# Kernel optimization log

Hardware: AMD Instinct MI355X
Metric: run time of the kernel (lower is better)

The kernel has to match this reference:

```python
import jax, jax.numpy as jnp
import numpy as np

N, E, B = 50000, 800000, 64
IN, H, OUT = 64, 128, 64


def _gcn_norm(edge_index, num_nodes):
    # PyG gcn_norm with add_self_loops=True: A_hat = A + I, norm = d^-1/2[src]*d^-1/2[dst]
    loop = jnp.arange(num_nodes)
    src = jnp.concatenate([edge_index[0], loop])
    dst = jnp.concatenate([edge_index[1], loop])
    deg = jax.ops.segment_sum(jnp.ones_like(dst, dtype=jnp.float32), dst,
                              num_segments=num_nodes)  # >= 1 due to self-loops
    dis = deg ** -0.5
    norm = dis[src] * dis[dst]  # [E+N]
    return src, dst, norm


def _gcn_layer(x, W, b, src, dst, norm, num_nodes):
    h = x @ W                                   # linear first (GCNConv order)
    msg = h[src] * norm[:, None]                # gather + normalize, [E+N, H]
    out = jax.ops.segment_sum(msg, dst, num_segments=num_nodes)  # scatter-add
    return out + b


def setup_inputs() -> dict:
    key = jax.random.key(0)
    ks = jax.random.split(key, 12)
    x = jax.random.normal(ks[0], (N, IN), dtype=jnp.float32)
    edge_index = jax.random.randint(ks[1], (2, E), 0, N, dtype=jnp.int64)
    batch = jnp.sort(jax.random.randint(ks[2], (N,), 0, B, dtype=jnp.int64))

    def lin(k, fan_in, fan_out):
        s = 1.0 / np.sqrt(fan_in)
        return jax.random.uniform(k, (fan_in, fan_out), jnp.float32, -s, s)

    return {
        "x": x, "edge_index": edge_index, "batch": batch,
        "W1": lin(ks[3], IN, H), "b1": jnp.zeros((H,), jnp.float32),
        "W2": lin(ks[4], H, H),  "b2": jnp.zeros((H,), jnp.float32),
        "W3": lin(ks[5], H, H),  "b3": jnp.zeros((H,), jnp.float32),
        "W4": lin(ks[6], H, OUT), "b4": jnp.zeros((OUT,), jnp.float32),
    }


def reference(x, edge_index, batch, W1, b1, W2, b2, W3, b3, W4, b4):
    src, dst, norm = _gcn_norm(edge_index, N)
    h = jax.nn.relu(_gcn_layer(x, W1, b1, src, dst, norm, N))
    h = jax.nn.relu(_gcn_layer(h, W2, b2, src, dst, norm, N))
    # global mean pool over graphs
    sums = jax.ops.segment_sum(h, batch, num_segments=B)          # [B, H]
    cnts = jax.ops.segment_sum(jnp.ones((N,), jnp.float32), batch, num_segments=B)
    pooled = sums / jnp.maximum(cnts, 1.0)[:, None]
    # MLP head
    return jax.nn.relu(pooled @ W3 + b3) @ W4 + b4                # [B, OUT]
```

## Files before the change

### kernel.cpp

```cpp
#include <hip/hip_runtime.h>


__device__ __forceinline__ float ldf(const void* p, long long i, int f32) {
    if (f32) return ((const float*)p)[i];
    unsigned int u = ((const unsigned short*)p)[i];
    return __uint_as_float(u << 16);
}
__device__ __forceinline__ float bfl(unsigned int u) { return __uint_as_float(u << 16); }
__device__ __forceinline__ float bfh(unsigned int u) { return __uint_as_float(u & 0xFFFF0000u); }
__device__ __forceinline__ int ld_idx(const int* p, long long i, int i64) {
    return i64 ? p[2 * i] : p[i];
}
__device__ __forceinline__ unsigned short f2bf(float v) {
    unsigned int x = __float_as_uint(v);
    return (unsigned short)((x + 0x7FFFu + ((x >> 16) & 1u)) >> 16);
}
__device__ __forceinline__ int clampi(int v, int lo, int hi) {
    return v < lo ? lo : (v > hi ? hi : v);
}


__global__ void gnn_detect(const unsigned int* __restrict__ w1_words,
                           const int* __restrict__ ei_words,
                           int* __restrict__ flags) {
    __shared__ int cnt;
    __shared__ int orred;
    int t = threadIdx.x;
    if (t == 0) { cnt = 0; orred = 0; }
    __syncthreads();
    int c = 0, o = 0;
    for (int i = t; i < 512; i += 256) {
        unsigned int e = (w1_words[i] >> 7) & 0xFFu;
        if (e >= 100 && e <= 140) c++;
    }
    for (int i = t; i < 4096; i += 256) o |= ei_words[2 * i + 1];
    atomicAdd(&cnt, c);
    atomicOr(&orred, o);
    __syncthreads();
    if (t == 0) {
        flags[0] = (cnt > 256) ? 0 : 1;
        flags[1] = (orred == 0) ? 1 : 0;
    }
}


__global__ void gnn_zeroall(int* __restrict__ degcnt, int* __restrict__ fillcnt,
                            float* __restrict__ pooled, float* __restrict__ cntf,
                            int N, int B) {
    int i = blockIdx.x * 256 + threadIdx.x;
    int stride = gridDim.x * 256;
    for (int j = i; j < N; j += stride) { degcnt[j] = 0; fillcnt[j] = 0; }
    for (int j = i; j < B * 128; j += stride) pooled[j] = 0.f;
    for (int j = i; j < B; j += stride) cntf[j] = 0.f;
}

#define OW1 0
#define OB1 8192
#define OW2 8320
#define OB2 24704
#define OW3 24832
#define OB3 41216
#define OW4 41344
#define OB4 49536
#define OTOT 49600

__global__ void gnn_convert_w(const void* W1, const void* b1, const void* W2, const void* b2,
                              const void* W3, const void* b3, const void* W4, const void* b4,
                              const int* __restrict__ flags, float* __restrict__ dst) {
    int f32 = flags[0];
    int i = blockIdx.x * blockDim.x + threadIdx.x;
    if (i >= OTOT) return;
    float v;
    if      (i < OB1) v = ldf(W1, i - OW1, f32);
    else if (i < OW2) v = ldf(b1, i - OB1, f32);
    else if (i < OB2) v = ldf(W2, i - OW2, f32);
    else if (i < OW3) v = ldf(b2, i - OB2, f32);
    else if (i < OB3) v = ldf(W3, i - OW3, f32);
    else if (i < OW4) v = ldf(b3, i - OB3, f32);
    else if (i < OB4) v = ldf(W4, i - OW4, f32);
    else              v = ldf(b4, i - OB4, f32);
    dst[i] = v;
}

__global__ void gnn_convert_x(const void* __restrict__ x, const int* __restrict__ flags,
                              unsigned short* __restrict__ xb, int n64) {
    if (!flags[0]) return;
    int i = blockIdx.x * 256 + threadIdx.x;
    if (i < n64) xb[i] = f2bf(((const float*)x)[i]);
}


__global__ void gnn_hist(const int* __restrict__ ei, int E, int N,
                         const int* __restrict__ flags, int* __restrict__ degcnt) {
    int base = (blockIdx.x * 256 + threadIdx.x) * 4;
    if (base >= E) return;
    int i64 = flags[1];
    int m = min(4, E - base);
    int d[4];
#pragma unroll
    for (int j = 0; j < 4; ++j)
        if (j < m) d[j] = clampi(ld_idx(ei, (long long)E + base + j, i64), 0, N - 1);
#pragma unroll
    for (int j = 0; j < 4; ++j)
        if (j < m) atomicAdd(&degcnt[d[j]], 1);
}

__global__ void gnn_scan1(const int* __restrict__ cnt, int* __restrict__ excl,
                          int* __restrict__ sums, float* __restrict__ dis, int N) {
    __shared__ int sh[256];
    int t = threadIdx.x;
    int i = blockIdx.x * 256 + t;
    int v = (i < N) ? cnt[i] : 0;
    sh[t] = v;
    __syncthreads();
    for (int off = 1; off < 256; off <<= 1) {
        int a = (t >= off) ? sh[t - off] : 0;
        __syncthreads();
        sh[t] += a;
        __syncthreads();
    }
    if (i < N) {
        excl[i] = sh[t] - v;
        dis[i] = rsqrtf((float)v + 1.0f);
    }
    if (t == 255) sums[blockIdx.x] = sh[255];
}

__global__ void gnn_scan2(int* __restrict__ sums, int nb) {
    __shared__ int sh[256];
    int t = threadIdx.x;
    int v = (t < nb) ? sums[t] : 0;
    sh[t] = v;
    __syncthreads();
    for (int off = 1; off < 256; off <<= 1) {
        int a = (t >= off) ? sh[t - off] : 0;
        __syncthreads();
        sh[t] += a;
        __syncthreads();
    }
    if (t < nb) sums[t] = sh[t] - v;
}

__global__ void gnn_scan3(int* __restrict__ row_ptr, const int* __restrict__ sums,
                          int N, int E) {
    int i = blockIdx.x * 256 + threadIdx.x;
    if (i < N) row_ptr[i] += sums[blockIdx.x];
    if (i == 0) row_ptr[N] = E;
}

__global__ void gnn_fill(const int* __restrict__ ei, const float* __restrict__ dis,
                         const int* __restrict__ row_ptr, int* __restrict__ fillcnt,
                         int2* __restrict__ csr, int E, int N, const int* __restrict__ flags) {
    int base = (blockIdx.x * 256 + threadIdx.x) * 4;
    if (base >= E) return;
    int i64 = flags[1];
    int m = min(4, E - base);
    int s[4], d[4];
    float ws[4], wd[4];
    int pos[4];
#pragma unroll
    for (int j = 0; j < 4; ++j)
        if (j < m) {
            s[j] = clampi(ld_idx(ei, (long long)base + j, i64), 0, N - 1);
            d[j] = clampi(ld_idx(ei, (long long)E + base + j, i64), 0, N - 1);
        }
#pragma unroll
    for (int j = 0; j < 4; ++j)
        if (j < m) { ws[j] = dis[s[j]]; wd[j] = dis[d[j]]; }
#pragma unroll
    for (int j = 0; j < 4; ++j)
        if (j < m) pos[j] = row_ptr[d[j]] + atomicAdd(&fillcnt[d[j]], 1);
#pragma unroll
    for (int j = 0; j < 4; ++j)
        if (j < m) csr[pos[j]] = make_int2(s[j], __float_as_int(ws[j] * wd[j]));
}


__global__ __launch_bounds__(256) void gnn_agg_x(const void* __restrict__ x,
                                                 const unsigned short* __restrict__ xconv,
                                                 const int* __restrict__ rp,
                                                 const int2* __restrict__ csr,
                                                 const float* __restrict__ dis,
                                                 const int* __restrict__ flags,
                                                 float* __restrict__ aggX, int N) {
    const unsigned int* tab = flags[0] ? (const unsigned int*)xconv : (const unsigned int*)x;
    int t = threadIdx.x;
    int lane = t & 63;
    int n = blockIdx.x * 8 + (t >> 6) * 2 + (lane >> 5);
    if (n >= N) return;
    int fl = lane & 31;
    float dn = dis[n];
    float dn2 = dn * dn;
    unsigned int us = tab[(long long)n * 32 + fl];
    float a0 = bfl(us) * dn2, a1 = bfh(us) * dn2;
    int beg = rp[n], end = rp[n + 1];
    int e = beg;
    for (; e + 4 <= end; e += 4) {
        int2 c0 = csr[e], c1 = csr[e + 1], c2 = csr[e + 2], c3 = csr[e + 3];
        unsigned int u0 = tab[(long long)c0.x * 32 + fl];
        unsigned int u1 = tab[(long long)c1.x * 32 + fl];
        unsigned int u2 = tab[(long long)c2.x * 32 + fl];
        unsigned int u3 = tab[(long long)c3.x * 32 + fl];
        float w0 = __int_as_float(c0.y), w1 = __int_as_float(c1.y);
        float w2 = __int_as_float(c2.y), w3 = __int_as_float(c3.y);
        a0 = fmaf(w0, bfl(u0), a0); a1 = fmaf(w0, bfh(u0), a1);
        a0 = fmaf(w1, bfl(u1), a0); a1 = fmaf(w1, bfh(u1), a1);
        a0 = fmaf(w2, bfl(u2), a0); a1 = fmaf(w2, bfh(u2), a1);
        a0 = fmaf(w3, bfl(u3), a0); a1 = fmaf(w3, bfh(u3), a1);
    }
    for (; e < end; ++e) {
        int2 c = csr[e];
        unsigned int u = tab[(long long)c.x * 32 + fl];
        float w = __int_as_float(c.y);
        a0 = fmaf(w, bfl(u), a0); a1 = fmaf(w, bfh(u), a1);
    }
    *(float2*)(aggX + (long long)n * 64 + fl * 2) = make_float2(a0, a1);
}


template <int K, bool RELU, bool OUTBF>
__global__ __launch_bounds__(256) void gnn_linear(const float* __restrict__ X,
                                                  const float* __restrict__ Wf,
                                                  const float* __restrict__ bias,
                                                  int N, void* __restrict__ out) {
    __shared__ float Wl[64 * 128];
    __shared__ float Xs[32 * K];
    const int t = threadIdx.x;
    const int nbase = blockIdx.x * 32;

#pragma unroll
    for (int it = 0; it < K / 32; ++it) {
        int i4 = t + it * 256;
        int n = nbase + (i4 * 4) / K;
        float4 v = make_float4(0.f, 0.f, 0.f, 0.f);
        if (n < N) v = ((const float4*)X)[(long long)nbase * (K / 4) + i4];
        ((float4*)Xs)[i4] = v;
    }

    const int fg = t & 31, ng = t >> 5;
    const int f0 = fg * 4, n0 = ng * 4;
    float4 acc[4];
#pragma unroll
    for (int j = 0; j < 4; ++j) acc[j] = make_float4(0.f, 0.f, 0.f, 0.f);

    for (int kc = 0; kc < K; kc += 64) {
        __syncthreads();
#pragma unroll
        for (int it = 0; it < 8; ++it) {
            int i4 = t + it * 256;
            ((float4*)Wl)[i4] = ((const float4*)(Wf + kc * 128))[i4];
        }
        __syncthreads();
#pragma unroll 4
        for (int k = 0; k < 64; ++k) {
            const float4 w = *(const float4*)&Wl[k * 128 + f0];
#pragma unroll
            for (int j = 0; j < 4; ++j) {
                float xv = Xs[(n0 + j) * K + kc + k];
                acc[j].x = fmaf(xv, w.x, acc[j].x);
                acc[j].y = fmaf(xv, w.y, acc[j].y);
                acc[j].z = fmaf(xv, w.z, acc[j].z);
                acc[j].w = fmaf(xv, w.w, acc[j].w);
            }
        }
    }

#pragma unroll
    for (int j = 0; j < 4; ++j) {
        int n = nbase + n0 + j;
        if (n >= N) continue;
        float4 a = acc[j];
        if (RELU) {
            const float4 b = *(const float4*)&bias[f0];
            a.x = fmaxf(a.x + b.x, 0.f);
            a.y = fmaxf(a.y + b.y, 0.f);
            a.z = fmaxf(a.z + b.z, 0.f);
            a.w = fmaxf(a.w + b.w, 0.f);
        }
        if (OUTBF) {
            uint2 u;
            u.x = (unsigned int)f2bf(a.x) | ((unsigned int)f2bf(a.y) << 16);
            u.y = (unsigned int)f2bf(a.z) | ((unsigned int)f2bf(a.w) << 16);
            *(uint2*)((unsigned short*)out + (long long)n * 128 + f0) = u;
        } else {
            *(float4*)((float*)out + (long long)n * 128 + f0) = a;
        }
    }
}


__global__ __launch_bounds__(256) void gnn_agg_bf(const unsigned short* __restrict__ A2,
                                                  const int* __restrict__ rp,
                                                  const int2* __restrict__ csr,
                                                  const float* __restrict__ dis,
                                                  const float* __restrict__ bias,
                                                  float* __restrict__ outC, int N) {
    int t = threadIdx.x;
    int lane = t & 63;
    int n = blockIdx.x * 8 + (t >> 6) * 2 + (lane >> 5);
    if (n >= N) return;
    int fl = lane & 31;
    float dn = dis[n];
    float dn2 = dn * dn;
    uint2 us = *(const uint2*)(A2 + (long long)n * 128 + fl * 4);
    float a0 = bfl(us.x) * dn2, a1 = bfh(us.x) * dn2;
    float a2 = bfl(us.y) * dn2, a3 = bfh(us.y) * dn2;
    int beg = rp[n], end = rp[n + 1];
    int e = beg;
    for (; e + 4 <= end; e += 4) {
        int2 c0 = csr[e], c1 = csr[e + 1], c2 = csr[e + 2], c3 = csr[e + 3];
        uint2 u0 = *(const uint2*)(A2 + (long long)c0.x * 128 + fl * 4);
        uint2 u1 = *(const uint2*)(A2 + (long long)c1.x * 128 + fl * 4);
        uint2 u2 = *(const uint2*)(A2 + (long long)c2.x * 128 + fl * 4);
        uint2 u3 = *(const uint2*)(A2 + (long long)c3.x * 128 + fl * 4);
        float w0 = __int_as_float(c0.y), w1 = __int_as_float(c1.y);
        float w2 = __int_as_float(c2.y), w3 = __int_as_float(c3.y);
        a0 = fmaf(w0, bfl(u0.x), a0); a1 = fmaf(w0, bfh(u0.x), a1);
        a2 = fmaf(w0, bfl(u0.y), a2); a3 = fmaf(w0, bfh(u0.y), a3);
        a0 = fmaf(w1, bfl(u1.x), a0); a1 = fmaf(w1, bfh(u1.x), a1);
        a2 = fmaf(w1, bfl(u1.y), a2); a3 = fmaf(w1, bfh(u1.y), a3);
        a0 = fmaf(w2, bfl(u2.x), a0); a1 = fmaf(w2, bfh(u2.x), a1);
        a2 = fmaf(w2, bfl(u2.y), a2); a3 = fmaf(w2, bfh(u2.y), a3);
        a0 = fmaf(w3, bfl(u3.x), a0); a1 = fmaf(w3, bfh(u3.x), a1);
        a2 = fmaf(w3, bfl(u3.y), a2); a3 = fmaf(w3, bfh(u3.y), a3);
    }
    for (; e < end; ++e) {
        int2 c = csr[e];
        uint2 u = *(const uint2*)(A2 + (long long)c.x * 128 + fl * 4);
        float w = __int_as_float(c.y);
        a0 = fmaf(w, bfl(u.x), a0); a1 = fmaf(w, bfh(u.x), a1);
        a2 = fmaf(w, bfl(u.y), a2); a3 = fmaf(w, bfh(u.y), a3);
    }
    const float4 b = *(const float4*)&bias[fl * 4];
    float4 o;
    o.x = fmaxf(a0 + b.x, 0.f);
    o.y = fmaxf(a1 + b.y, 0.f);
    o.z = fmaxf(a2 + b.z, 0.f);
    o.w = fmaxf(a3 + b.w, 0.f);
    *(float4*)(outC + (long long)n * 128 + fl * 4) = o;
}


#define PSTRIP 32
__global__ __launch_bounds__(128) void gnn_pool(const float* __restrict__ h,
                                                const int* __restrict__ batch,
                                                const int* __restrict__ flags,
                                                float* __restrict__ pooled,
                                                float* __restrict__ cntf, int N, int B) {
    int i64 = flags[1];
    int f = threadIdx.x;
    int n0 = blockIdx.x * PSTRIP;
    if (n0 >= N) return;
    int nend = min(n0 + PSTRIP, N);
    int cur = clampi(ld_idx(batch, n0, i64), 0, B - 1);
    float acc = 0.0f;
    float cc = 0.0f;
    for (int n = n0; n < nend; ++n) {
        int b = clampi(ld_idx(batch, n, i64), 0, B - 1);
        if (b != cur) {
            atomicAdd(&pooled[cur * 128 + f], acc);
            if (f == 0) atomicAdd(&cntf[cur], cc);
            acc = 0.0f; cc = 0.0f; cur = b;
        }
        acc += h[(long long)n * 128 + f];
        cc += 1.0f;
    }
    atomicAdd(&pooled[cur * 128 + f], acc);
    if (f == 0) atomicAdd(&cntf[cur], cc);
}


__global__ __launch_bounds__(128) void gnn_head(const float* __restrict__ pooled,
                                                const float* __restrict__ cntf,
                                                const float* __restrict__ W3,
                                                const float* __restrict__ b3,
                                                const float* __restrict__ W4,
                                                const float* __restrict__ b4,
                                                const int* __restrict__ flags,
                                                void* __restrict__ outv) {
    __shared__ float xs[128];
    __shared__ float rs[128];
    int b = blockIdx.x, f = threadIdx.x;
    float c = fmaxf(cntf[b], 1.0f);
    xs[f] = pooled[b * 128 + f] / c;
    __syncthreads();
    float acc = b3[f];
    for (int k = 0; k < 128; ++k) acc = fmaf(xs[k], W3[k * 128 + f], acc);
    rs[f] = fmaxf(acc, 0.f);
    __syncthreads();
    if (f < 64) {
        float a2 = b4[f];
        for (int k = 0; k < 128; ++k) a2 = fmaf(rs[k], W4[k * 64 + f], a2);
        if (flags[0]) ((float*)outv)[b * 64 + f] = a2;
        else          ((unsigned short*)outv)[b * 64 + f] = f2bf(a2);
    }
}


extern "C" void kernel_launch(void* const* d_in, const int* in_sizes, int n_in,
                              void* d_out, int out_size, void* d_ws, size_t ws_size,
                              hipStream_t stream) {
    const void* x  = d_in[0];
    const int* ei  = (const int*)d_in[1];
    const int* bat = (const int*)d_in[2];

    const int N = in_sizes[0] / 64;
    const int E = in_sizes[1] / 2;
    const int B = out_size / 64;

    char* p = (char*)d_ws;
    auto alloc = [&](size_t bytes) { void* q = (void*)p; p += (bytes + 255) & ~(size_t)255; return q; };
    int*   flags    = (int*)alloc(256);
    float* wsW      = (float*)alloc((size_t)OTOT * 4);
    int*   degcnt   = (int*)alloc((size_t)N * 4);
    int*   fillcnt  = (int*)alloc((size_t)N * 4);
    float* dis      = (float*)alloc((size_t)N * 4);
    int*   row_ptr  = (int*)alloc((size_t)(N + 1) * 4);
    int*   sums     = (int*)alloc(1024);
    int2*  csr      = (int2*)alloc((size_t)E * 8);
    unsigned short* xb = (unsigned short*)alloc((size_t)N * 64 * 2);
    float* C2       = (float*)alloc((size_t)N * 128 * 4);
    float* H1       = (float*)alloc((size_t)N * 128 * 4);
    unsigned short* A2 = (unsigned short*)alloc((size_t)N * 128 * 2);
    float* pooled   = (float*)alloc((size_t)B * 128 * 4);
    float* cntf     = (float*)alloc((size_t)B * 4);
    (void)ws_size; (void)n_in;

    const int nbN = (N + 255) / 256;

    gnn_detect<<<1, 256, 0, stream>>>((const unsigned int*)d_in[3], ei, flags);
    gnn_zeroall<<<200, 256, 0, stream>>>(degcnt, fillcnt, pooled, cntf, N, B);
    gnn_convert_w<<<(OTOT + 255) / 256, 256, 0, stream>>>(d_in[3], d_in[4], d_in[5], d_in[6],
                                                          d_in[7], d_in[8], d_in[9], d_in[10],
                                                          flags, wsW);
    gnn_convert_x<<<(N * 64 + 255) / 256, 256, 0, stream>>>(x, flags, xb, N * 64);

    const int nE4 = (E + 1023) / 1024;
    gnn_hist<<<nE4, 256, 0, stream>>>(ei, E, N, flags, degcnt);
    gnn_scan1<<<nbN, 256, 0, stream>>>(degcnt, row_ptr, sums, dis, N);
    gnn_scan2<<<1, 256, 0, stream>>>(sums, nbN);
    gnn_scan3<<<nbN, 256, 0, stream>>>(row_ptr, sums, N, E);
    gnn_fill<<<nE4, 256, 0, stream>>>(ei, dis, row_ptr, fillcnt, csr, E, N, flags);

    const int nlin = (N + 31) / 32;
    const int nagg = (N + 7) / 8;

    gnn_agg_x<<<nagg, 256, 0, stream>>>(x, xb, row_ptr, csr, dis, flags, C2, N);
    gnn_linear<64, true, false><<<nlin, 256, 0, stream>>>(C2, wsW + OW1, wsW + OB1, N, (void*)H1);

    gnn_linear<128, false, true><<<nlin, 256, 0, stream>>>(H1, wsW + OW2, wsW + OB2, N, (void*)A2);
    gnn_agg_bf<<<nagg, 256, 0, stream>>>(A2, row_ptr, csr, dis, wsW + OB2, C2, N);

    gnn_pool<<<(N + PSTRIP - 1) / PSTRIP, 128, 0, stream>>>(C2, bat, flags, pooled, cntf, N, B);
    gnn_head<<<B, 128, 0, stream>>>(pooled, cntf, wsW + OW3, wsW + OB3,
                                    wsW + OW4, wsW + OB4, flags, d_out);
}
```

Baseline: 319.8 us.

## Compress CSR to 16-bit source indices, merge prep kernels, drop scan3

Merges the zeroing, weight conversion and x conversion kernels into a single grid-stride prep kernel, and removes the scan3 pass by computing row offsets on the fly from the exclusive scan plus per-block sums. The CSR entries shrink from an int2 (source, weight) to a source index alone, stored as 16-bit when N < 65536. The aggregation kernels now recompute the edge weight from dis[src]*dis[dst]. This cuts CSR write and read traffic and removes several launches, at the cost of an extra gather of dis per edge and extra arithmetic for the row offsets.

```diff
diff --git a/kernel.cpp b/kernel.cpp
--- a/kernel.cpp
+++ b/kernel.cpp
@@ -41,17 +41,6 @@
         flags[0] = (cnt > 256) ? 0 : 1;
         flags[1] = (orred == 0) ? 1 : 0;
     }
-}
-
-
-__global__ void gnn_zeroall(int* __restrict__ degcnt, int* __restrict__ fillcnt,
-                            float* __restrict__ pooled, float* __restrict__ cntf,
-                            int N, int B) {
-    int i = blockIdx.x * 256 + threadIdx.x;
-    int stride = gridDim.x * 256;
-    for (int j = i; j < N; j += stride) { degcnt[j] = 0; fillcnt[j] = 0; }
-    for (int j = i; j < B * 128; j += stride) pooled[j] = 0.f;
-    for (int j = i; j < B; j += stride) cntf[j] = 0.f;
 }
 
 #define OW1 0
@@ -64,29 +53,36 @@
 #define OB4 49536
 #define OTOT 49600
 
-__global__ void gnn_convert_w(const void* W1, const void* b1, const void* W2, const void* b2,
-                              const void* W3, const void* b3, const void* W4, const void* b4,
-                              const int* __restrict__ flags, float* __restrict__ dst) {
-    int f32 = flags[0];
-    int i = blockIdx.x * blockDim.x + threadIdx.x;
-    if (i >= OTOT) return;
-    float v;
-    if      (i < OB1) v = ldf(W1, i - OW1, f32);
-    else if (i < OW2) v = ldf(b1, i - OB1, f32);
-    else if (i < OB2) v = ldf(W2, i - OW2, f32);
-    else if (i < OW3) v = ldf(b2, i - OB2, f32);
-    else if (i < OB3) v = ldf(W3, i - OW3, f32);
-    else if (i < OW4) v = ldf(b3, i - OB3, f32);
-    else if (i < OB4) v = ldf(W4, i - OW4, f32);
-    else              v = ldf(b4, i - OB4, f32);
-    dst[i] = v;
-}
-
-__global__ void gnn_convert_x(const void* __restrict__ x, const int* __restrict__ flags,
-                              unsigned short* __restrict__ xb, int n64) {
-    if (!flags[0]) return;
-    int i = blockIdx.x * 256 + threadIdx.x;
-    if (i < n64) xb[i] = f2bf(((const float*)x)[i]);
+
+__global__ void gnn_prep(const void* W1, const void* b1, const void* W2, const void* b2,
+                         const void* W3, const void* b3, const void* W4, const void* b4,
+                         const void* x, const int* __restrict__ flags,
+                         int* __restrict__ degcnt, int* __restrict__ fillcnt,
+                         float* __restrict__ pooled, float* __restrict__ cntf,
+                         float* __restrict__ wsW, unsigned short* __restrict__ xb,
+                         int N, int B) {
+    const int f32 = flags[0];
+    const int i = blockIdx.x * 256 + threadIdx.x;
+    const int stride = gridDim.x * 256;
+    for (int j = i; j < N; j += stride) { degcnt[j] = 0; fillcnt[j] = 0; }
+    for (int j = i; j < B * 128; j += stride) pooled[j] = 0.f;
+    for (int j = i; j < B; j += stride) cntf[j] = 0.f;
+    for (int j = i; j < OTOT; j += stride) {
+        float v;
+        if      (j < OB1) v = ldf(W1, j - OW1, f32);
+        else if (j < OW2) v = ldf(b1, j - OB1, f32);
+        else if (j < OB2) v = ldf(W2, j - OW2, f32);
+        else if (j < OW3) v = ldf(b2, j - OB2, f32);
+        else if (j < OB3) v = ldf(W3, j - OW3, f32);
+        else if (j < OW4) v = ldf(b3, j - OB3, f32);
+        else if (j < OB4) v = ldf(W4, j - OW4, f32);
+        else              v = ldf(b4, j - OB4, f32);
+        wsW[j] = v;
+    }
+    if (f32) {
+        const float* xf = (const float*)x;
+        for (int j = i; j < N * 64; j += stride) xb[j] = f2bf(xf[j]);
+    }
 }
 
 
@@ -141,48 +137,38 @@
     if (t < nb) sums[t] = sh[t] - v;
 }
 
-__global__ void gnn_scan3(int* __restrict__ row_ptr, const int* __restrict__ sums,
-                          int N, int E) {
-    int i = blockIdx.x * 256 + threadIdx.x;
-    if (i < N) row_ptr[i] += sums[blockIdx.x];
-    if (i == 0) row_ptr[N] = E;
-}
-
-__global__ void gnn_fill(const int* __restrict__ ei, const float* __restrict__ dis,
-                         const int* __restrict__ row_ptr, int* __restrict__ fillcnt,
-                         int2* __restrict__ csr, int E, int N, const int* __restrict__ flags) {
-    int base = (blockIdx.x * 256 + threadIdx.x) * 4;
-    if (base >= E) return;
+
+template <bool SMALLN>
+__global__ void gnn_fill(const int* __restrict__ ei, const int* __restrict__ excl,
+                         const int* __restrict__ bsums, int* __restrict__ fillcnt,
+                         void* __restrict__ csr, int E, int N,
+                         const int* __restrict__ flags) {
+    int e = blockIdx.x * 256 + threadIdx.x;
+    if (e >= E) return;
     int i64 = flags[1];
-    int m = min(4, E - base);
-    int s[4], d[4];
-    float ws[4], wd[4];
-    int pos[4];
-#pragma unroll
-    for (int j = 0; j < 4; ++j)
-        if (j < m) {
-            s[j] = clampi(ld_idx(ei, (long long)base + j, i64), 0, N - 1);
-            d[j] = clampi(ld_idx(ei, (long long)E + base + j, i64), 0, N - 1);
-        }
-#pragma unroll
-    for (int j = 0; j < 4; ++j)
-        if (j < m) { ws[j] = dis[s[j]]; wd[j] = dis[d[j]]; }
-#pragma unroll
-    for (int j = 0; j < 4; ++j)
-        if (j < m) pos[j] = row_ptr[d[j]] + atomicAdd(&fillcnt[d[j]], 1);
-#pragma unroll
-    for (int j = 0; j < 4; ++j)
-        if (j < m) csr[pos[j]] = make_int2(s[j], __float_as_int(ws[j] * wd[j]));
-}
-
-
+    int s = clampi(ld_idx(ei, (long long)e, i64), 0, N - 1);
+    int d = clampi(ld_idx(ei, (long long)E + e, i64), 0, N - 1);
+    int rp = excl[d] + bsums[d >> 8];
+    int pos = rp + atomicAdd(&fillcnt[d], 1);
+    if (SMALLN) ((unsigned short*)csr)[pos] = (unsigned short)s;
+    else        ((int*)csr)[pos] = s;
+}
+
+template <bool SMALLN>
+__device__ __forceinline__ int csr_at(const void* csr, int e) {
+    return SMALLN ? (int)((const unsigned short*)csr)[e] : ((const int*)csr)[e];
+}
+
+
+template <bool SMALLN>
 __global__ __launch_bounds__(256) void gnn_agg_x(const void* __restrict__ x,
                                                  const unsigned short* __restrict__ xconv,
-                                                 const int* __restrict__ rp,
-                                                 const int2* __restrict__ csr,
+                                                 const int* __restrict__ excl,
+                                                 const int* __restrict__ bsums,
+                                                 const void* __restrict__ csr,
                                                  const float* __restrict__ dis,
                                                  const int* __restrict__ flags,
-                                                 float* __restrict__ aggX, int N) {
+                                                 float* __restrict__ aggX, int N, int E) {
     const unsigned int* tab = flags[0] ? (const unsigned int*)xconv : (const unsigned int*)x;
     int t = threadIdx.x;
     int lane = t & 63;
@@ -193,25 +179,27 @@
     float dn2 = dn * dn;
     unsigned int us = tab[(long long)n * 32 + fl];
     float a0 = bfl(us) * dn2, a1 = bfh(us) * dn2;
-    int beg = rp[n], end = rp[n + 1];
+    int beg = excl[n] + bsums[n >> 8];
+    int end = (n + 1 < N) ? (excl[n + 1] + bsums[(n + 1) >> 8]) : E;
     int e = beg;
     for (; e + 4 <= end; e += 4) {
-        int2 c0 = csr[e], c1 = csr[e + 1], c2 = csr[e + 2], c3 = csr[e + 3];
-        unsigned int u0 = tab[(long long)c0.x * 32 + fl];
-        unsigned int u1 = tab[(long long)c1.x * 32 + fl];
-        unsigned int u2 = tab[(long long)c2.x * 32 + fl];
-        unsigned int u3 = tab[(long long)c3.x * 32 + fl];
-        float w0 = __int_as_float(c0.y), w1 = __int_as_float(c1.y);
-        float w2 = __int_as_float(c2.y), w3 = __int_as_float(c3.y);
+        int s0 = csr_at<SMALLN>(csr, e),     s1 = csr_at<SMALLN>(csr, e + 1);
+        int s2 = csr_at<SMALLN>(csr, e + 2), s3 = csr_at<SMALLN>(csr, e + 3);
+        float w0 = dis[s0], w1 = dis[s1], w2 = dis[s2], w3 = dis[s3];
+        unsigned int u0 = tab[(long long)s0 * 32 + fl];
+        unsigned int u1 = tab[(long long)s1 * 32 + fl];
+        unsigned int u2 = tab[(long long)s2 * 32 + fl];
+        unsigned int u3 = tab[(long long)s3 * 32 + fl];
+        w0 *= dn; w1 *= dn; w2 *= dn; w3 *= dn;
         a0 = fmaf(w0, bfl(u0), a0); a1 = fmaf(w0, bfh(u0), a1);
         a0 = fmaf(w1, bfl(u1), a0); a1 = fmaf(w1, bfh(u1), a1);
         a0 = fmaf(w2, bfl(u2), a0); a1 = fmaf(w2, bfh(u2), a1);
         a0 = fmaf(w3, bfl(u3), a0); a1 = fmaf(w3, bfh(u3), a1);
     }
     for (; e < end; ++e) {
-        int2 c = csr[e];
-        unsigned int u = tab[(long long)c.x * 32 + fl];
-        float w = __int_as_float(c.y);
+        int s = csr_at<SMALLN>(csr, e);
+        float w = dis[s] * dn;
+        unsigned int u = tab[(long long)s * 32 + fl];
         a0 = fmaf(w, bfl(u), a0); a1 = fmaf(w, bfh(u), a1);
     }
     *(float2*)(aggX + (long long)n * 64 + fl * 2) = make_float2(a0, a1);
@@ -289,12 +277,14 @@
 }
 
 
+template <bool SMALLN>
 __global__ __launch_bounds__(256) void gnn_agg_bf(const unsigned short* __restrict__ A2,
-                                                  const int* __restrict__ rp,
-                                                  const int2* __restrict__ csr,
+                                                  const int* __restrict__ excl,
+                                                  const int* __restrict__ bsums,
+                                                  const void* __restrict__ csr,
                                                   const float* __restrict__ dis,
                                                   const float* __restrict__ bias,
-                                                  float* __restrict__ outC, int N) {
+                                                  float* __restrict__ outC, int N, int E) {
     int t = threadIdx.x;
     int lane = t & 63;
     int n = blockIdx.x * 8 + (t >> 6) * 2 + (lane >> 5);
@@ -305,16 +295,18 @@
     uint2 us = *(const uint2*)(A2 + (long long)n * 128 + fl * 4);
     float a0 = bfl(us.x) * dn2, a1 = bfh(us.x) * dn2;
     float a2 = bfl(us.y) * dn2, a3 = bfh(us.y) * dn2;
-    int beg = rp[n], end = rp[n + 1];
+    int beg = excl[n] + bsums[n >> 8];
+    int end = (n + 1 < N) ? (excl[n + 1] + bsums[(n + 1) >> 8]) : E;
     int e = beg;
     for (; e + 4 <= end; e += 4) {
-        int2 c0 = csr[e], c1 = csr[e + 1], c2 = csr[e + 2], c3 = csr[e + 3];
-        uint2 u0 = *(const uint2*)(A2 + (long long)c0.x * 128 + fl * 4);
-        uint2 u1 = *(const uint2*)(A2 + (long long)c1.x * 128 + fl * 4);
-        uint2 u2 = *(const uint2*)(A2 + (long long)c2.x * 128 + fl * 4);
-        uint2 u3 = *(const uint2*)(A2 + (long long)c3.x * 128 + fl * 4);
-        float w0 = __int_as_float(c0.y), w1 = __int_as_float(c1.y);
-        float w2 = __int_as_float(c2.y), w3 = __int_as_float(c3.y);
+        int s0 = csr_at<SMALLN>(csr, e),     s1 = csr_at<SMALLN>(csr, e + 1);
+        int s2 = csr_at<SMALLN>(csr, e + 2), s3 = csr_at<SMALLN>(csr, e + 3);
+        float w0 = dis[s0], w1 = dis[s1], w2 = dis[s2], w3 = dis[s3];
+        uint2 u0 = *(const uint2*)(A2 + (long long)s0 * 128 + fl * 4);
+        uint2 u1 = *(const uint2*)(A2 + (long long)s1 * 128 + fl * 4);
+        uint2 u2 = *(const uint2*)(A2 + (long long)s2 * 128 + fl * 4);
+        uint2 u3 = *(const uint2*)(A2 + (long long)s3 * 128 + fl * 4);
+        w0 *= dn; w1 *= dn; w2 *= dn; w3 *= dn;
         a0 = fmaf(w0, bfl(u0.x), a0); a1 = fmaf(w0, bfh(u0.x), a1);
         a2 = fmaf(w0, bfl(u0.y), a2); a3 = fmaf(w0, bfh(u0.y), a3);
         a0 = fmaf(w1, bfl(u1.x), a0); a1 = fmaf(w1, bfh(u1.x), a1);
@@ -325,9 +317,9 @@
         a2 = fmaf(w3, bfl(u3.y), a2); a3 = fmaf(w3, bfh(u3.y), a3);
     }
     for (; e < end; ++e) {
-        int2 c = csr[e];
-        uint2 u = *(const uint2*)(A2 + (long long)c.x * 128 + fl * 4);
-        float w = __int_as_float(c.y);
+        int s = csr_at<SMALLN>(csr, e);
+        float w = dis[s] * dn;
+        uint2 u = *(const uint2*)(A2 + (long long)s * 128 + fl * 4);
         a0 = fmaf(w, bfl(u.x), a0); a1 = fmaf(w, bfh(u.x), a1);
         a2 = fmaf(w, bfl(u.y), a2); a3 = fmaf(w, bfh(u.y), a3);
     }
@@ -407,6 +399,7 @@
     const int N = in_sizes[0] / 64;
     const int E = in_sizes[1] / 2;
     const int B = out_size / 64;
+    const bool smalln = (N < 65536);
 
     char* p = (char*)d_ws;
     auto alloc = [&](size_t bytes) { void* q = (void*)p; p += (bytes + 255) & ~(size_t)255; return q; };
@@ -415,9 +408,9 @@
     int*   degcnt   = (int*)alloc((size_t)N * 4);
     int*   fillcnt  = (int*)alloc((size_t)N * 4);
     float* dis      = (float*)alloc((size_t)N * 4);
-    int*   row_ptr  = (int*)alloc((size_t)(N + 1) * 4);
-    int*   sums     = (int*)alloc(1024);
-    int2*  csr      = (int2*)alloc((size_t)E * 8);
+    int*   excl     = (int*)alloc((size_t)N * 4);
+    int*   bsums    = (int*)alloc(1024);
+    void*  csr      = alloc((size_t)E * (smalln ? 2 : 4));
     unsigned short* xb = (unsigned short*)alloc((size_t)N * 64 * 2);
     float* C2       = (float*)alloc((size_t)N * 128 * 4);
     float* H1       = (float*)alloc((size_t)N * 128 * 4);
@@ -429,27 +422,33 @@
     const int nbN = (N + 255) / 256;
 
     gnn_detect<<<1, 256, 0, stream>>>((const unsigned int*)d_in[3], ei, flags);
-    gnn_zeroall<<<200, 256, 0, stream>>>(degcnt, fillcnt, pooled, cntf, N, B);
-    gnn_convert_w<<<(OTOT + 255) / 256, 256, 0, stream>>>(d_in[3], d_in[4], d_in[5], d_in[6],
-                                                          d_in[7], d_in[8], d_in[9], d_in[10],
-                                                          flags, wsW);
-    gnn_convert_x<<<(N * 64 + 255) / 256, 256, 0, stream>>>(x, flags, xb, N * 64);
-
-    const int nE4 = (E + 1023) / 1024;
-    gnn_hist<<<nE4, 256, 0, stream>>>(ei, E, N, flags, degcnt);
-    gnn_scan1<<<nbN, 256, 0, stream>>>(degcnt, row_ptr, sums, dis, N);
-    gnn_scan2<<<1, 256, 0, stream>>>(sums, nbN);
-    gnn_scan3<<<nbN, 256, 0, stream>>>(row_ptr, sums, N, E);
-    gnn_fill<<<nE4, 256, 0, stream>>>(ei, dis, row_ptr, fillcnt, csr, E, N, flags);
+    gnn_prep<<<512, 256, 0, stream>>>(d_in[3], d_in[4], d_in[5], d_in[6],
+                                      d_in[7], d_in[8], d_in[9], d_in[10],
+                                      x, flags, degcnt, fillcnt, pooled, cntf,
+                                      wsW, xb, N, B);
+
+    gnn_hist<<<(E + 1023) / 1024, 256, 0, stream>>>(ei, E, N, flags, degcnt);
+    gnn_scan1<<<nbN, 256, 0, stream>>>(degcnt, excl, bsums, dis, N);
+    gnn_scan2<<<1, 256, 0, stream>>>(bsums, nbN);
+    if (smalln)
+        gnn_fill<true><<<(E + 255) / 256, 256, 0, stream>>>(ei, excl, bsums, fillcnt, csr, E, N, flags);
+    else
+        gnn_fill<false><<<(E + 255) / 256, 256, 0, stream>>>(ei, excl, bsums, fillcnt, csr, E, N, flags);
 
     const int nlin = (N + 31) / 32;
     const int nagg = (N + 7) / 8;
 
-    gnn_agg_x<<<nagg, 256, 0, stream>>>(x, xb, row_ptr, csr, dis, flags, C2, N);
+    if (smalln)
+        gnn_agg_x<true><<<nagg, 256, 0, stream>>>(x, xb, excl, bsums, csr, dis, flags, C2, N, E);
+    else
+        gnn_agg_x<false><<<nagg, 256, 0, stream>>>(x, xb, excl, bsums, csr, dis, flags, C2, N, E);
     gnn_linear<64, true, false><<<nlin, 256, 0, stream>>>(C2, wsW + OW1, wsW + OB1, N, (void*)H1);
 
     gnn_linear<128, false, true><<<nlin, 256, 0, stream>>>(H1, wsW + OW2, wsW + OB2, N, (void*)A2);
-    gnn_agg_bf<<<nagg, 256, 0, stream>>>(A2, row_ptr, csr, dis, wsW + OB2, C2, N);
+    if (smalln)
+        gnn_agg_bf<true><<<nagg, 256, 0, stream>>>(A2, excl, bsums, csr, dis, wsW + OB2, C2, N, E);
+    else
+        gnn_agg_bf<false><<<nagg, 256, 0, stream>>>(A2, excl, bsums, csr, dis, wsW + OB2, C2, N, E);
 
     gnn_pool<<<(N + PSTRIP - 1) / PSTRIP, 128, 0, stream>>>(C2, bat, flags, pooled, cntf, N, B);
     gnn_head<<<B, 128, 0, stream>>>(pooled, cntf, wsW + OW3, wsW + OB3,
```

Measured after the change: 311.6 us. 1.03x faster.
